# Kernel optimization log

Hardware: AMD Instinct MI355X
Metric: run time of the kernel (lower is better)

## Reference

```python
import jax, jax.numpy as jnp
import numpy as np

RADIUS = 4        # config.corr_radius
NUM_LEVELS = 4    # config.corr_levels
EPS = 1e-12       # F.normalize eps


def _avg_pool(x, s):
    # F.avg_pool2d(x, s, stride=s) for H,W divisible by s
    if s == 1:
        return x
    B, C, H, W = x.shape
    return x.reshape(B, C, H // s, s, W // s, s).mean(axis=(3, 5))


def _l2_normalize(x):
    # F.normalize(x, dim=1): x / max(||x||_2, eps)
    n = jnp.sqrt(jnp.sum(x * x, axis=1, keepdims=True))
    return x / jnp.maximum(n, EPS)


def _correlation(f1, f2, r=RADIUS):
    # windowed local correlation: corr[dy,dx](y,x) = sum_c f1(y,x) * f2(y-dy, x-dx)
    B, C, H, W = f1.shape
    f1 = _l2_normalize(f1)
    f2 = _l2_normalize(f2)
    f2p = jnp.pad(f2, ((0, 0), (0, 0), (r, r), (r, r)))  # zero pad = zero fill outside
    corrs = []
    for dy in range(-r, r + 1):
        for dx in range(-r, r + 1):
            sh = jax.lax.slice(f2p, (0, 0, r - dy, r - dx), (B, C, r - dy + H, r - dx + W))
            corrs.append(jnp.sum(f1 * sh, axis=1))  # [B,H,W]
    return jnp.stack(corrs, axis=1)  # [B, (2r+1)^2, H, W]


def setup_inputs() -> dict:
    key = jax.random.key(0)
    k1, k2, k3, k4 = jax.random.split(key, 4)
    B, C, H, W = 4, 256, 128, 192
    return {
        "fmap1": jax.random.normal(k1, (B, C, H, W), jnp.float32),
        "fmap2": jax.random.normal(k2, (B, C, H, W), jnp.float32),
        "depth1": jax.random.uniform(k3, (B, 1, H, W), jnp.float32),
        "depth2": jax.random.uniform(k4, (B, 1, H, W), jnp.float32),
        "depth_weight": jnp.asarray(0.1, jnp.float32),
    }


def reference(fmap1, fmap2, depth1, depth2, depth_weight):
    pyramid = []
    for i in range(NUM_LEVELS):
        s = 2 ** i
        corr = _correlation(_avg_pool(fmap1, s), _avg_pool(fmap2, s))
        # depth correlation enhancement: exp(-|d1 - d2|), broadcast over 81 channels
        dd = jnp.abs(_avg_pool(depth1, s) - _avg_pool(depth2, s))  # [B,1,h,w]
        corr = corr + depth_weight * jnp.exp(-dd)
        pyramid.append(corr)
    return tuple(pyramid)
```

## Files before the change

kernel.cpp:

```cpp
#include <hip/hip_runtime.h>
#include <hip/hip_bf16.h>

typedef __attribute__((ext_vector_type(8))) __bf16 bf16x8;
typedef __attribute__((ext_vector_type(4))) float f32x4;
typedef unsigned short ushort_t;
typedef unsigned int uint_t;

#define CCH 256
#define BB 4

#define NP32_0 3145728
#define NP32_1 786432
#define NP32_2 196608
#define NP32_3 49152

__device__ __forceinline__ ushort_t f2b(float v) {
    __hip_bfloat16 h = __float2bfloat16(v);
    return *reinterpret_cast<ushort_t*>(&h);
}

__device__ __forceinline__ void gload16(const void* g, void* l) {
    __builtin_amdgcn_global_load_lds(
        (const __attribute__((address_space(1))) void*)g,
        (__attribute__((address_space(3))) void*)l, 16, 0, 0);
}

struct PrepPtrs {
    ushort_t* o0; ushort_t* o1; ushort_t* o2; ushort_t* o3;
    float* n0; float* n1; float* n2; float* n3;
};

__global__ __launch_bounds__(256, 3) void pyr_prep_kernel(
    const float* __restrict__ fa, const float* __restrict__ fb,
    PrepPtrs Pa, PrepPtrs Pb)
{
    const int H = 128, W = 192;
    const int HW = H * W;
    const float* fin = blockIdx.y ? fb : fa;
    PrepPtrs P = blockIdx.y ? Pb : Pa;

    __shared__ float lds0[32 * 260];
    __shared__ float lds1[32 * 68];
    __shared__ float lds2[32 * 20];
    __shared__ float red[256];

    int xc = blockIdx.x % 6;
    int ys = (blockIdx.x / 6) % 16;
    int b  = blockIdx.x / 96;
    int gx0 = xc * 32, gy0 = ys * 8;
    int t = threadIdx.x;

    const float* gsrc[8];
    int lofs[8];
    #pragma unroll
    for (int j = 0; j < 8; ++j) {
        int e = t + 256 * j;
        int c = e >> 6, r = (e >> 3) & 7, x4 = e & 7;
        gsrc[j] = fin + ((size_t)(b * 256 + c) * H + gy0 + r) * W + gx0 + 4 * x4;
        lofs[j] = c * 260 + r * 32 + 4 * x4;
    }

    float4 stg[8];
    auto issue = [&](int kc) {
        #pragma unroll
        for (int j = 0; j < 8; ++j)
            stg[j] = *reinterpret_cast<const float4*>(gsrc[j] + (size_t)kc * (32 * HW));
    };

    float ssq0 = 0.f, ssq1 = 0.f, ssq2 = 0.f, ssq3 = 0.f;

    size_t p0g = (size_t)(b * H + gy0 + (t >> 5)) * W + gx0 + (t & 31);
    int wv = t >> 6, q = t & 63, qy = q >> 4, qx = q & 15;
    size_t l1g = (size_t)(b * 64 + ys * 4 + qy) * 96 + xc * 16 + qx;
    int cb2 = t >> 4, sI = t & 15, sy2 = sI >> 3, sx2 = sI & 7;
    size_t l2g = (size_t)(b * 32 + ys * 2 + sy2) * 48 + xc * 8 + sx2;
    int cb3 = t >> 2, u3 = t & 3;
    size_t l3g = (size_t)(b * 16 + ys) * 24 + xc * 4 + u3;

    issue(0);
    #pragma unroll 1
    for (int kc = 0; kc < 8; ++kc) {
        #pragma unroll
        for (int j = 0; j < 8; ++j)
            *reinterpret_cast<float4*>(&lds0[lofs[j]]) = stg[j];
        if (kc < 7) issue(kc + 1);
        __syncthreads();

        {
            uint_t uu[16];
            #pragma unroll
            for (int i = 0; i < 16; ++i) {
                float va = lds0[(2 * i) * 260 + t];
                float vb = lds0[(2 * i + 1) * 260 + t];
                ssq0 = fmaf(va, va, ssq0);
                ssq0 = fmaf(vb, vb, ssq0);
                uu[i] = (uint_t)f2b(va) | ((uint_t)f2b(vb) << 16);
            }
            ushort_t* dst = P.o0 + (size_t)kc * NP32_0 + p0g * 32;
            *reinterpret_cast<uint4*>(dst +  0) = make_uint4(uu[0],  uu[1],  uu[2],  uu[3]);
            *reinterpret_cast<uint4*>(dst +  8) = make_uint4(uu[4],  uu[5],  uu[6],  uu[7]);
            *reinterpret_cast<uint4*>(dst + 16) = make_uint4(uu[8],  uu[9],  uu[10], uu[11]);
            *reinterpret_cast<uint4*>(dst + 24) = make_uint4(uu[12], uu[13], uu[14], uu[15]);
        }

        {
            float a8[8];
            #pragma unroll
            for (int h = 0; h < 8; ++h) {
                int c = wv * 8 + h;
                float2 s0 = *reinterpret_cast<const float2*>(&lds0[c * 260 + (2 * qy) * 32 + 2 * qx]);
                float2 s1 = *reinterpret_cast<const float2*>(&lds0[c * 260 + (2 * qy + 1) * 32 + 2 * qx]);
                a8[h] = 0.25f * (s0.x + s0.y + s1.x + s1.y);
                ssq1 = fmaf(a8[h], a8[h], ssq1);
            }
            uint_t vv[4];
            #pragma unroll
            for (int i = 0; i < 4; ++i)
                vv[i] = (uint_t)f2b(a8[2 * i]) | ((uint_t)f2b(a8[2 * i + 1]) << 16);
            *reinterpret_cast<uint4*>(P.o1 + (size_t)kc * NP32_1 + l1g * 32 + wv * 8)
                = make_uint4(vv[0], vv[1], vv[2], vv[3]);
            #pragma unroll
            for (int h = 0; h < 8; ++h)
                lds1[(wv * 8 + h) * 68 + q] = a8[h];
        }
        __syncthreads();

        if (t < 128) {
            float a4[4];
            #pragma unroll
            for (int cc = 0; cc < 4; ++cc) {
                int c = cb2 * 4 + cc;
                float2 s0 = *reinterpret_cast<const float2*>(&lds1[c * 68 + (2 * sy2) * 16 + 2 * sx2]);
                float2 s1 = *reinterpret_cast<const float2*>(&lds1[c * 68 + (2 * sy2 + 1) * 16 + 2 * sx2]);
                a4[cc] = 0.25f * (s0.x + s0.y + s1.x + s1.y);
                ssq2 = fmaf(a4[cc], a4[cc], ssq2);
            }
            uint_t w0 = (uint_t)f2b(a4[0]) | ((uint_t)f2b(a4[1]) << 16);
            uint_t w1 = (uint_t)f2b(a4[2]) | ((uint_t)f2b(a4[3]) << 16);
            *reinterpret_cast<uint2*>(P.o2 + (size_t)kc * NP32_2 + l2g * 32 + cb2 * 4) = make_uint2(w0, w1);
            #pragma unroll
            for (int cc = 0; cc < 4; ++cc)
                lds2[(cb2 * 4 + cc) * 20 + sI] = a4[cc];
        }
        __syncthreads();

        if (t < 32) {
            float a4[4];
            #pragma unroll
            for (int cc = 0; cc < 4; ++cc) {
                int c = cb3 * 4 + cc;
                float2 s0 = *reinterpret_cast<const float2*>(&lds2[c * 20 + 2 * u3]);
                float2 s1 = *reinterpret_cast<const float2*>(&lds2[c * 20 + 8 + 2 * u3]);
                a4[cc] = 0.25f * (s0.x + s0.y + s1.x + s1.y);
                ssq3 = fmaf(a4[cc], a4[cc], ssq3);
            }
            uint_t w0 = (uint_t)f2b(a4[0]) | ((uint_t)f2b(a4[1]) << 16);
            uint_t w1 = (uint_t)f2b(a4[2]) | ((uint_t)f2b(a4[3]) << 16);
            *reinterpret_cast<uint2*>(P.o3 + (size_t)kc * NP32_3 + l3g * 32 + cb3 * 4) = make_uint2(w0, w1);
        }
    }

    P.n0[p0g] = 1.f / fmaxf(sqrtf(ssq0), 1e-12f);
    red[t] = ssq1;
    __syncthreads();
    if (t < 64) {
        float sm = red[t] + red[t + 64] + red[t + 128] + red[t + 192];
        P.n1[(size_t)(b * 64 + ys * 4 + (t >> 4)) * 96 + xc * 16 + (t & 15)]
            = 1.f / fmaxf(sqrtf(sm), 1e-12f);
    }
    __syncthreads();
    if (t < 128) red[t] = ssq2;
    __syncthreads();
    if (t < 16) {
        float sm = 0.f;
        #pragma unroll
        for (int c = 0; c < 8; ++c) sm += red[t + 16 * c];
        P.n2[(size_t)(b * 32 + ys * 2 + (t >> 3)) * 48 + xc * 8 + (t & 7)]
            = 1.f / fmaxf(sqrtf(sm), 1e-12f);
    }
    __syncthreads();
    if (t < 32) red[t] = ssq3;
    __syncthreads();
    if (t < 4) {
        float sm = 0.f;
        #pragma unroll
        for (int c = 0; c < 8; ++c) sm += red[t + 4 * c];
        P.n3[(size_t)(b * 16 + ys) * 24 + xc * 4 + t]
            = 1.f / fmaxf(sqrtf(sm), 1e-12f);
    }
}

__global__ __launch_bounds__(256, 2) void corr_mfma2_kernel(
    const ushort_t* __restrict__ f1n, const ushort_t* __restrict__ f2n,
    const float* __restrict__ invn1, const float* __restrict__ invn2,
    const float* __restrict__ dt, float* __restrict__ out,
    const ushort_t* __restrict__ zblk, int H, int W, int TX, int TY, int npix32)
{
    __shared__ char smem[65536];
    char* As = smem;
    char* Bs = smem + 16384;

    int bid = blockIdx.x;
    int cpx = gridDim.x >> 3;
    int swz = (bid & 7) * cpx + (bid >> 3);
    int tx = swz % TX;
    int ty = (swz / TX) % TY;
    int b  = swz / (TX * TY);
    int x0 = tx * 16, y0 = ty * 8;

    int tid = threadIdx.x;
    int w = tid >> 6, lane = tid & 63;
    int kg = lane >> 4, col = lane & 15;
    int r2 = col >> 2, c2 = col & 3;
    int sy = w >> 1, p = w & 1;

    const ushort_t* srcA[2]; char* ldsA[2];
    #pragma unroll
    for (int q = 0; q < 2; ++q) {
        int qq = w * 2 + q;
        int kgs = qq >> 1, reg = qq & 1;
        int slot = reg * 64 + lane;
        int ly = slot >> 4, lxp = slot & 15;
        int lx = lxp ^ (4 * (ly & 1));
        srcA[q] = f1n + ((size_t)((b * H + y0 + ly) * W) + x0 + lx) * 32 + kgs * 8;
        ldsA[q] = As + qq * 1024;
    }
    const ushort_t* srcB[6]; int advB[6]; char* ldsB[6];
    #pragma unroll
    for (int q = 0; q < 6; ++q) {
        int qq = w * 6 + q;
        int kgs = qq / 6, reg = qq % 6;
        int slot = reg * 64 + lane;
        int wy = slot / 24, wxp = slot % 24;
        int wx = wxp ^ (4 * (wy & 1));
        int py = y0 - 4 + wy, px = x0 - 4 + wx;
        bool v = (py >= 0) && (py < H) && (px >= 0) && (px < W);
        srcB[q] = v ? (f2n + ((size_t)((b * H + py) * W) + px) * 32 + kgs * 8) : zblk;
        advB[q] = v ? npix32 : 0;
        ldsB[q] = Bs + qq * 1024;
    }

    int aoff[2], boff[3][4];
    #pragma unroll
    for (int s = 0; s < 2; ++s) {
        int sxs = 2 * p + s;
        int ly = 4 * sy + r2;
        int lx = (4 * sxs + c2) ^ (4 * (ly & 1));
        aoff[s] = kg * 2048 + (ly * 16 + lx) * 16;
    }
    #pragma unroll
    for (int i = 0; i < 3; ++i)
        #pragma unroll
        for (int j = 0; j < 4; ++j) {
            int wy = 4 * (sy + i) + r2;
            int wx = (4 * (2 * p + j) + c2) ^ (4 * (wy & 1));
            boff[i][j] = kg * 6144 + (wy * 24 + wx) * 16;
        }

    f32x4 acc0[3][3] = {};
    f32x4 acc1[3][3] = {};

    #pragma unroll
    for (int q = 0; q < 2; ++q) { gload16(srcA[q], ldsA[q]); srcA[q] += npix32; }
    #pragma unroll
    for (int q = 0; q < 6; ++q) { gload16(srcB[q], ldsB[q]); srcB[q] += advB[q]; }

    int buf = 0;
    #pragma unroll 1
    for (int kc = 0; kc < 8; ++kc) {
        if (kc < 7) {
            int boA = (buf ^ 1) * 8192;
            int boB = (buf ^ 1) * 24576;
            #pragma unroll
            for (int q = 0; q < 2; ++q) { gload16(srcA[q], ldsA[q] + boA); srcA[q] += npix32; }
            #pragma unroll
            for (int q = 0; q < 6; ++q) { gload16(srcB[q], ldsB[q] + boB); srcB[q] += advB[q]; }
            __builtin_amdgcn_sched_barrier(0);
            asm volatile("s_waitcnt vmcnt(8)" ::: "memory");
        } else {
            __builtin_amdgcn_sched_barrier(0);
            asm volatile("s_waitcnt vmcnt(0)" ::: "memory");
        }
        __builtin_amdgcn_s_barrier();
        __builtin_amdgcn_sched_barrier(0);

        const char* Ab = As + buf * 8192;
        const char* Bb = Bs + buf * 24576;
        bf16x8 av0 = *(const bf16x8*)(Ab + aoff[0]);
        bf16x8 av1 = *(const bf16x8*)(Ab + aoff[1]);
        #pragma unroll
        for (int i = 0; i < 3; ++i) {
            #pragma unroll
            for (int j = 0; j < 4; ++j) {
                bf16x8 bv = *(const bf16x8*)(Bb + boff[i][j]);
                if (j < 3) acc0[i][j]     = __builtin_amdgcn_mfma_f32_16x16x32_bf16(av0, bv, acc0[i][j], 0, 0, 0);
                if (j > 0) acc1[i][j - 1] = __builtin_amdgcn_mfma_f32_16x16x32_bf16(av1, bv, acc1[i][j - 1], 0, 0, 0);
            }
        }
        if (kc < 7) {
            __builtin_amdgcn_sched_barrier(0);
            __builtin_amdgcn_s_barrier();
            __builtin_amdgcn_sched_barrier(0);
        }
        buf ^= 1;
    }

    float inv1v[2][4], dtv[2][4];
    #pragma unroll
    for (int s = 0; s < 2; ++s) {
        int sxs = 2 * p + s;
        #pragma unroll
        for (int rr = 0; rr < 4; ++rr) {
            int m = kg * 4 + rr;
            int iy = m >> 2, ix = m & 3;
            int pix = (b * H + y0 + 4 * sy + iy) * W + x0 + 4 * sxs + ix;
            inv1v[s][rr] = invn1[pix];
            dtv[s][rr]   = dt[pix];
        }
    }
    #pragma unroll
    for (int s = 0; s < 2; ++s) {
        int sxs = 2 * p + s;
        #pragma unroll
        for (int i = 0; i < 3; ++i) {
            #pragma unroll
            for (int jj = 0; jj < 3; ++jj) {
                int wy = 4 * (sy + i) + r2;
                int wxr = 4 * (sxs + jj) + c2;
                int py = y0 - 4 + wy, px = x0 - 4 + wxr;
                bool v = (py >= 0) && (py < H) && (px >= 0) && (px < W);
                float i2 = v ? invn2[(b * H + py) * W + px] : 0.f;
                f32x4 a = (s == 0) ? acc0[i][jj] : acc1[i][jj];
                #pragma unroll
                for (int rr = 0; rr < 4; ++rr) {
                    int m = kg * 4 + rr;
                    int iy = m >> 2, ix = m & 3;
                    int oy = iy + 8 - (4 * i + r2);
                    int ox = ix + 8 - (4 * jj + c2);
                    if (oy >= 0 && oy < 9 && ox >= 0 && ox < 9) {
                        int gy = y0 + 4 * sy + iy, gx = x0 + 4 * sxs + ix;
                        out[((size_t)(b * 81 + oy * 9 + ox) * H + gy) * W + gx]
                            = a[rr] * inv1v[s][rr] * i2 + dtv[s][rr];
                    }
                }
            }
        }
    }
}

__global__ __launch_bounds__(256) void corr_mfma_kernel(
    const ushort_t* __restrict__ f1n, const ushort_t* __restrict__ f2n,
    const float* __restrict__ invn1, const float* __restrict__ invn2,
    const float* __restrict__ dt, float* __restrict__ out,
    int H, int W, int TX, int TY, int zoff)
{
    int wid  = threadIdx.x >> 6;
    int lane = threadIdx.x & 63;
    int tile = blockIdx.x * 4 + wid;
    int ntiles = BB * TY * TX;
    if (tile >= ntiles) return;
    int tx = tile % TX;
    int ty = (tile / TX) % TY;
    int b  = tile / (TX * TY);
    int x0 = tx * 4, y0 = ty * 4;

    int col = lane & 15;
    int kg  = lane >> 4;

    int iyA = col >> 2, ixA = col & 3;
    int a_off = (((b * H + y0 + iyA) * W) + x0 + ixA) * 32 + kg * 8;

    int b_off[9], badv[9];
    uint_t vmask = 0;
    #pragma unroll
    for (int tt = 0; tt < 9; ++tt) {
        int w = tt * 16 + col;
        int wy = w / 12, wx = w % 12;
        int py = y0 + wy - 4, px = x0 + wx - 4;
        bool v = (py >= 0) && (py < H) && (px >= 0) && (px < W);
        b_off[tt] = v ? (((b * H + py) * W + px) * 32 + kg * 8) : (zoff + kg * 8);
        badv[tt] = v ? NP32_3 : 0;
        if (v) vmask |= (1u << tt);
    }

    f32x4 acc[9] = {};
    #pragma unroll
    for (int kb = 0; kb < 8; ++kb) {
        bf16x8 av = *reinterpret_cast<const bf16x8*>(f1n + a_off + kb * NP32_3);
        #pragma unroll
        for (int tt = 0; tt < 9; ++tt) {
            bf16x8 bv = *reinterpret_cast<const bf16x8*>(f2n + b_off[tt]);
            acc[tt] = __builtin_amdgcn_mfma_f32_16x16x32_bf16(av, bv, acc[tt], 0, 0, 0);
            b_off[tt] += badv[tt];
        }
    }

    float inv1[4], dts[4];
    #pragma unroll
    for (int r = 0; r < 4; ++r) {
        int m = kg * 4 + r;
        int iy = m >> 2, ix = m & 3;
        int pix = (b * H + y0 + iy) * W + x0 + ix;
        inv1[r] = invn1[pix];
        dts[r]  = dt[pix];
    }
    #pragma unroll
    for (int tt = 0; tt < 9; ++tt) {
        int w = tt * 16 + col;
        int wy = w / 12, wx = w % 12;
        int py = y0 + wy - 4, px = x0 + wx - 4;
        float i2 = ((vmask >> tt) & 1u) ? invn2[(b * H + py) * W + px] : 0.f;
        #pragma unroll
        for (int r = 0; r < 4; ++r) {
            int m = kg * 4 + r;
            int iy = m >> 2, ix = m & 3;
            int oy = iy + 8 - wy, ox = ix + 8 - wx;
            if (oy >= 0 && oy < 9 && ox >= 0 && ox < 9) {
                int o = oy * 9 + ox;
                out[((size_t)(b * 81 + o) * H + (y0 + iy)) * W + (x0 + ix)]
                    = acc[tt][r] * inv1[r] * i2 + dts[r];
            }
        }
    }
}

__global__ __launch_bounds__(256) void depth_kernel(
    const float* __restrict__ d1, const float* __restrict__ d2,
    const float* __restrict__ dw,
    float* __restrict__ dt0, float* __restrict__ dt1,
    float* __restrict__ dt2, float* __restrict__ dt3)
{
    int rid = blockIdx.x * 256 + threadIdx.x;
    if (rid >= 4 * 16 * 24) return;
    int b = rid / 384, rr = rid % 384, ry = rr / 24, rx = rr % 24;
    const int H = 128, W = 192;
    float w0 = dw[0];
    size_t base0 = ((size_t)b * H + ry * 8) * W + rx * 8;

    float q1[4][4], q2[4][4];
    #pragma unroll
    for (int yy = 0; yy < 4; ++yy) {
        float4 a0 = *reinterpret_cast<const float4*>(d1 + base0 + (2 * yy) * W);
        float4 a1 = *reinterpret_cast<const float4*>(d1 + base0 + (2 * yy) * W + 4);
        float4 a2 = *reinterpret_cast<const float4*>(d1 + base0 + (2 * yy + 1) * W);
        float4 a3 = *reinterpret_cast<const float4*>(d1 + base0 + (2 * yy + 1) * W + 4);
        float4 b0 = *reinterpret_cast<const float4*>(d2 + base0 + (2 * yy) * W);
        float4 b1 = *reinterpret_cast<const float4*>(d2 + base0 + (2 * yy) * W + 4);
        float4 b2 = *reinterpret_cast<const float4*>(d2 + base0 + (2 * yy + 1) * W);
        float4 b3 = *reinterpret_cast<const float4*>(d2 + base0 + (2 * yy + 1) * W + 4);
        float ra[2][8] = {{a0.x,a0.y,a0.z,a0.w,a1.x,a1.y,a1.z,a1.w},
                          {a2.x,a2.y,a2.z,a2.w,a3.x,a3.y,a3.z,a3.w}};
        float rb[2][8] = {{b0.x,b0.y,b0.z,b0.w,b1.x,b1.y,b1.z,b1.w},
                          {b2.x,b2.y,b2.z,b2.w,b3.x,b3.y,b3.z,b3.w}};
        #pragma unroll
        for (int e = 0; e < 2; ++e) {
            float o[8];
            #pragma unroll
            for (int xx = 0; xx < 8; ++xx) o[xx] = w0 * expf(-fabsf(ra[e][xx] - rb[e][xx]));
            *reinterpret_cast<float4*>(dt0 + base0 + (2 * yy + e) * W)     = make_float4(o[0], o[1], o[2], o[3]);
            *reinterpret_cast<float4*>(dt0 + base0 + (2 * yy + e) * W + 4) = make_float4(o[4], o[5], o[6], o[7]);
        }
        #pragma unroll
        for (int xx = 0; xx < 4; ++xx) {
            q1[yy][xx] = 0.25f * (ra[0][2 * xx] + ra[0][2 * xx + 1] + ra[1][2 * xx] + ra[1][2 * xx + 1]);
            q2[yy][xx] = 0.25f * (rb[0][2 * xx] + rb[0][2 * xx + 1] + rb[1][2 * xx] + rb[1][2 * xx + 1]);
        }
    }
    #pragma unroll
    for (int yy = 0; yy < 4; ++yy)
        #pragma unroll
        for (int xx = 0; xx < 4; ++xx)
            dt1[((size_t)b * 64 + ry * 4 + yy) * 96 + rx * 4 + xx] = w0 * expf(-fabsf(q1[yy][xx] - q2[yy][xx]));

    float r1[2][2], r2m[2][2];
    #pragma unroll
    for (int y = 0; y < 2; ++y)
        #pragma unroll
        for (int x = 0; x < 2; ++x) {
            r1[y][x]  = 0.25f * (q1[2 * y][2 * x] + q1[2 * y][2 * x + 1] + q1[2 * y + 1][2 * x] + q1[2 * y + 1][2 * x + 1]);
            r2m[y][x] = 0.25f * (q2[2 * y][2 * x] + q2[2 * y][2 * x + 1] + q2[2 * y + 1][2 * x] + q2[2 * y + 1][2 * x + 1]);
            dt2[((size_t)b * 32 + ry * 2 + y) * 48 + rx * 2 + x] = w0 * expf(-fabsf(r1[y][x] - r2m[y][x]));
        }
    float s1 = 0.25f * (r1[0][0] + r1[0][1] + r1[1][0] + r1[1][1]);
    float s2 = 0.25f * (r2m[0][0] + r2m[0][1] + r2m[1][0] + r2m[1][1]);
    dt3[((size_t)b * 16 + ry) * 24 + rx] = w0 * expf(-fabsf(s1 - s2));
}

extern "C" void kernel_launch(void* const* d_in, const int* in_sizes, int n_in,
                              void* d_out, int out_size, void* d_ws, size_t ws_size,
                              hipStream_t stream) {
    const float* f1 = (const float*)d_in[0];
    const float* f2 = (const float*)d_in[1];
    const float* d1 = (const float*)d_in[2];
    const float* d2 = (const float*)d_in[3];
    const float* dw = (const float*)d_in[4];
    float* out = (float*)d_out;
    float* ws  = (float*)d_ws;

    size_t o = 0;
    float* in1_0 = ws + o; o += (size_t)4 * 128 * 192;
    float* in1_1 = ws + o; o += (size_t)4 * 64 * 96;
    float* in1_2 = ws + o; o += (size_t)4 * 32 * 48;
    float* in1_3 = ws + o; o += (size_t)4 * 16 * 24;
    float* in2_0 = ws + o; o += (size_t)4 * 128 * 192;
    float* in2_1 = ws + o; o += (size_t)4 * 64 * 96;
    float* in2_2 = ws + o; o += (size_t)4 * 32 * 48;
    float* in2_3 = ws + o; o += (size_t)4 * 16 * 24;
    float* dt_0 = ws + o; o += (size_t)4 * 128 * 192;
    float* dt_1 = ws + o; o += (size_t)4 * 64 * 96;
    float* dt_2 = ws + o; o += (size_t)4 * 32 * 48;
    float* dt_3 = ws + o; o += (size_t)4 * 16 * 24;
    o = (o + 7) & ~(size_t)7;

    ushort_t* sws = (ushort_t*)(ws + o);
    const size_t L0 = (size_t)4 * 128 * 192 * 256;
    const size_t L1 = (size_t)4 * 64 * 96 * 256;
    const size_t L2 = (size_t)4 * 32 * 48 * 256;
    const size_t L3 = (size_t)4 * 16 * 24 * 256;
    const size_t FT = L0 + L1 + L2 + L3;
    ushort_t* f1n0 = sws;
    ushort_t* f1n1 = f1n0 + L0;
    ushort_t* f1n2 = f1n1 + L1;
    ushort_t* f1n3 = f1n2 + L2;
    ushort_t* f2n0 = sws + FT;
    ushort_t* f2n1 = f2n0 + L0;
    ushort_t* f2n2 = f2n1 + L1;
    ushort_t* f2n3 = f2n2 + L2;
    ushort_t* zblk = sws + 2 * FT;
    size_t need = o * 4 + (2 * FT + 256) * 2;
    if (ws_size < need) return;

    hipMemsetAsync(zblk, 0, 512, stream);

    depth_kernel<<<dim3(6), 256, 0, stream>>>(d1, d2, dw, dt_0, dt_1, dt_2, dt_3);

    PrepPtrs Pa = { f1n0, f1n1, f1n2, f1n3, in1_0, in1_1, in1_2, in1_3 };
    PrepPtrs Pb = { f2n0, f2n1, f2n2, f2n3, in2_0, in2_1, in2_2, in2_3 };
    pyr_prep_kernel<<<dim3(384, 2), 256, 0, stream>>>(f1, f2, Pa, Pb);

    corr_mfma2_kernel<<<dim3(16 * 12 * 4), 256, 0, stream>>>(f1n0, f2n0, in1_0, in2_0, dt_0, out,           zblk, 128, 192, 12, 16, NP32_0);
    corr_mfma2_kernel<<<dim3( 8 *  6 * 4), 256, 0, stream>>>(f1n1, f2n1, in1_1, in2_1, dt_1, out + 7962624, zblk,  64,  96,  6,  8, NP32_1);
    corr_mfma2_kernel<<<dim3( 4 *  3 * 4), 256, 0, stream>>>(f1n2, f2n2, in1_2, in2_2, dt_2, out + 9953280, zblk,  32,  48,  3,  4, NP32_2);
    corr_mfma_kernel<<<dim3(96 / 4), 256, 0, stream>>>(f1n3, f2n3, in1_3, in2_3, dt_3, out + 10450944, 16, 24, 6, 4,
                                                       (int)(2 * FT - (size_t)(f2n3 - sws)));
}
```

Measured before the change: 276.7 us.

## Fuse three correlation level launches into one kernel and re-swizzle LDS layout

Replaces three separate launches of the tiled MFMA correlation kernel, one per pyramid level, with a single 1008-block launch that picks its level from the block index. This removes launch gaps and lets the small levels share the GPU with the tail of level 0. It also changes the LDS tile layout from channel-group-major with a row-parity XOR to pixel-major with a per-pixel XOR swizzle on the 16-byte channel chunk. The global load mapping changes to match, and the zero block is now indexed per chunk. The goal is better coalescing and fewer LDS bank conflicts, at the risk of a layout mismatch or uneven block scheduling across levels.

Result: faster. 241.2 us (-12.8%).

```diff
diff --git a/kernel.cpp b/kernel.cpp
--- a/kernel.cpp
+++ b/kernel.cpp
@@ -190,19 +190,30 @@
     }
 }
 
-__global__ __launch_bounds__(256, 2) void corr_mfma2_kernel(
-    const ushort_t* __restrict__ f1n, const ushort_t* __restrict__ f2n,
-    const float* __restrict__ invn1, const float* __restrict__ invn2,
-    const float* __restrict__ dt, float* __restrict__ out,
-    const ushort_t* __restrict__ zblk, int H, int W, int TX, int TY, int npix32)
+struct CorrLvl {
+    const ushort_t* f1n; const ushort_t* f2n;
+    const float* in1; const float* in2; const float* dt;
+    float* out;
+    int H, W, TX, TY, npix32;
+};
+
+__global__ __launch_bounds__(256, 2) void corr_fused_kernel(
+    CorrLvl Lv0, CorrLvl Lv1, CorrLvl Lv2, const ushort_t* __restrict__ zblk)
 {
     __shared__ char smem[65536];
     char* As = smem;
     char* Bs = smem + 16384;
 
     int bid = blockIdx.x;
-    int cpx = gridDim.x >> 3;
-    int swz = (bid & 7) * cpx + (bid >> 3);
+    CorrLvl L;
+    int local;
+    if (bid < 768)      { L = Lv0; local = bid; }
+    else if (bid < 960) { L = Lv1; local = bid - 768; }
+    else                { L = Lv2; local = bid - 960; }
+
+    int H = L.H, W = L.W, TX = L.TX, TY = L.TY, npix32 = L.npix32;
+    int cpx = (BB * TX * TY) >> 3;
+    int swz = (local & 7) * cpx + (local >> 3);
     int tx = swz % TX;
     int ty = (swz / TX) % TY;
     int b  = swz / (TX * TY);
@@ -213,48 +224,45 @@
     int kg = lane >> 4, col = lane & 15;
     int r2 = col >> 2, c2 = col & 3;
     int sy = w >> 1, p = w & 1;
+    int kgx = kg ^ c2;
 
     const ushort_t* srcA[2]; char* ldsA[2];
     #pragma unroll
     for (int q = 0; q < 2; ++q) {
-        int qq = w * 2 + q;
-        int kgs = qq >> 1, reg = qq & 1;
-        int slot = reg * 64 + lane;
-        int ly = slot >> 4, lxp = slot & 15;
-        int lx = lxp ^ (4 * (ly & 1));
-        srcA[q] = f1n + ((size_t)((b * H + y0 + ly) * W) + x0 + lx) * 32 + kgs * 8;
-        ldsA[q] = As + qq * 1024;
+        int row = w * 2 + q;
+        int px = lane >> 2, js = lane & 3;
+        int j = js ^ (px & 3);
+        srcA[q] = L.f1n + ((size_t)((b * H + y0 + row) * W) + x0 + px) * 32 + j * 8;
+        ldsA[q] = As + row * 1024;
     }
     const ushort_t* srcB[6]; int advB[6]; char* ldsB[6];
     #pragma unroll
     for (int q = 0; q < 6; ++q) {
-        int qq = w * 6 + q;
-        int kgs = qq / 6, reg = qq % 6;
-        int slot = reg * 64 + lane;
-        int wy = slot / 24, wxp = slot % 24;
-        int wx = wxp ^ (4 * (wy & 1));
-        int py = y0 - 4 + wy, px = x0 - 4 + wx;
-        bool v = (py >= 0) && (py < H) && (px >= 0) && (px < W);
-        srcB[q] = v ? (f2n + ((size_t)((b * H + py) * W) + px) * 32 + kgs * 8) : zblk;
+        int u = (w * 6 + q) * 64 + lane;
+        int row = u / 96, rem = u % 96;
+        int px = rem >> 2, js = rem & 3;
+        int j = js ^ (px & 3);
+        int py = y0 - 4 + row, pxg = x0 - 4 + px;
+        bool v = (py >= 0) && (py < H) && (pxg >= 0) && (pxg < W);
+        srcB[q] = v ? (L.f2n + ((size_t)((b * H + py) * W) + pxg) * 32 + j * 8) : (zblk + j * 8);
         advB[q] = v ? npix32 : 0;
-        ldsB[q] = Bs + qq * 1024;
+        ldsB[q] = Bs + (w * 6 + q) * 1024;
     }
 
     int aoff[2], boff[3][4];
     #pragma unroll
     for (int s = 0; s < 2; ++s) {
-        int sxs = 2 * p + s;
         int ly = 4 * sy + r2;
-        int lx = (4 * sxs + c2) ^ (4 * (ly & 1));
-        aoff[s] = kg * 2048 + (ly * 16 + lx) * 16;
+        int lx = 4 * (2 * p + s) + c2;
+        aoff[s] = ((ly * 16 + lx) * 4 + kgx) * 16;
     }
     #pragma unroll
     for (int i = 0; i < 3; ++i)
         #pragma unroll
         for (int j = 0; j < 4; ++j) {
             int wy = 4 * (sy + i) + r2;
-            int wx = (4 * (2 * p + j) + c2) ^ (4 * (wy & 1));
-            boff[i][j] = kg * 6144 + (wy * 24 + wx) * 16;
+            int wx = 4 * (2 * p + j) + c2;
+            boff[i][j] = ((wy * 24 + wx) * 4 + kgx) * 16;
         }
 
     f32x4 acc0[3][3] = {};
@@ -314,8 +322,8 @@
             int m = kg * 4 + rr;
             int iy = m >> 2, ix = m & 3;
             int pix = (b * H + y0 + 4 * sy + iy) * W + x0 + 4 * sxs + ix;
-            inv1v[s][rr] = invn1[pix];
-            dtv[s][rr]   = dt[pix];
+            inv1v[s][rr] = L.in1[pix];
+            dtv[s][rr]   = L.dt[pix];
         }
     }
     #pragma unroll
@@ -329,7 +337,7 @@
                 int wxr = 4 * (sxs + jj) + c2;
                 int py = y0 - 4 + wy, px = x0 - 4 + wxr;
                 bool v = (py >= 0) && (py < H) && (px >= 0) && (px < W);
-                float i2 = v ? invn2[(b * H + py) * W + px] : 0.f;
+                float i2 = v ? L.in2[(b * H + py) * W + px] : 0.f;
                 f32x4 a = (s == 0) ? acc0[i][jj] : acc1[i][jj];
                 #pragma unroll
                 for (int rr = 0; rr < 4; ++rr) {
@@ -339,7 +347,7 @@
                     int ox = ix + 8 - (4 * jj + c2);
                     if (oy >= 0 && oy < 9 && ox >= 0 && ox < 9) {
                         int gy = y0 + 4 * sy + iy, gx = x0 + 4 * sxs + ix;
-                        out[((size_t)(b * 81 + oy * 9 + ox) * H + gy) * W + gx]
+                        L.out[((size_t)(b * 81 + oy * 9 + ox) * H + gy) * W + gx]
                             = a[rr] * inv1v[s][rr] * i2 + dtv[s][rr];
                     }
                 }
@@ -538,9 +546,11 @@
     PrepPtrs Pb = { f2n0, f2n1, f2n2, f2n3, in2_0, in2_1, in2_2, in2_3 };
     pyr_prep_kernel<<<dim3(384, 2), 256, 0, stream>>>(f1, f2, Pa, Pb);
 
-    corr_mfma2_kernel<<<dim3(16 * 12 * 4), 256, 0, stream>>>(f1n0, f2n0, in1_0, in2_0, dt_0, out,           zblk, 128, 192, 12, 16, NP32_0);
-    corr_mfma2_kernel<<<dim3( 8 *  6 * 4), 256, 0, stream>>>(f1n1, f2n1, in1_1, in2_1, dt_1, out + 7962624, zblk,  64,  96,  6,  8, NP32_1);
-    corr_mfma2_kernel<<<dim3( 4 *  3 * 4), 256, 0, stream>>>(f1n2, f2n2, in1_2, in2_2, dt_2, out + 9953280, zblk,  32,  48,  3,  4, NP32_2);
+    CorrLvl lv0 = { f1n0, f2n0, in1_0, in2_0, dt_0, out,           128, 192, 12, 16, NP32_0 };
+    CorrLvl lv1 = { f1n1, f2n1, in1_1, in2_1, dt_1, out + 7962624,  64,  96,  6,  8, NP32_1 };
+    CorrLvl lv2 = { f1n2, f2n2, in1_2, in2_2, dt_2, out + 9953280,  32,  48,  3,  4, NP32_2 };
+    corr_fused_kernel<<<dim3(1008), 256, 0, stream>>>(lv0, lv1, lv2, zblk);
+
     corr_mfma_kernel<<<dim3(96 / 4), 256, 0, stream>>>(f1n3, f2n3, in1_3, in2_3, dt_3, out + 10450944, 16, 24, 6, 4,
                                                        (int)(2 * FT - (size_t)(f2n3 - sws)));
 }
```
